# Optimization experiments

Measured on AMD Instinct MI355X. Metric: run time of the kernel, lower is better.

Reference implementation:

```python
import jax, jax.numpy as jnp
import numpy as np

N_EMBD = 1024
N_HEAD = 16
HEAD_DIM = N_EMBD // N_HEAD


def setup_inputs() -> dict:
    key = jax.random.key(0)
    ks = jax.random.split(key, 9)
    B, T, C = 4, 2048, N_EMBD
    s = 1.0 / np.sqrt(C)
    return {
        "x": jax.random.normal(ks[0], (B, T, C), dtype=jnp.float32),
        "Wq": jax.random.normal(ks[1], (C, C), dtype=jnp.float32) * s,
        "bq": jnp.zeros((C,), dtype=jnp.float32),
        "Wk": jax.random.normal(ks[2], (C, C), dtype=jnp.float32) * s,
        "bk": jnp.zeros((C,), dtype=jnp.float32),
        "Wv": jax.random.normal(ks[3], (C, C), dtype=jnp.float32) * s,
        "bv": jnp.zeros((C,), dtype=jnp.float32),
        "Wo": jax.random.normal(ks[4], (C, C), dtype=jnp.float32) * s,
        "bo": jnp.zeros((C,), dtype=jnp.float32),
    }


def reference(x, Wq, bq, Wk, bk, Wv, bv, Wo, bo):
    B, T, C = x.shape
    H, D = N_HEAD, HEAD_DIM
    # torch Linear: y = x @ W.T + b ; here W stored as (in, out) so y = x @ W + b
    q = (x @ Wq + bq).reshape(B, T, H, D).transpose(0, 2, 1, 3)  # [B,H,T,D]
    k = (x @ Wk + bk).reshape(B, T, H, D).transpose(0, 2, 1, 3)
    v = (x @ Wv + bv).reshape(B, T, H, D).transpose(0, 2, 1, 3)
    scores = jnp.einsum('bhqd,bhkd->bhqk', q, k) / jnp.sqrt(jnp.float32(D))
    causal = jnp.tril(jnp.ones((T, T), dtype=bool))  # [T,T]
    scores = jnp.where(causal[None, None, :, :], scores, -jnp.inf)
    weights = jax.nn.softmax(scores, axis=-1)
    # dropout disabled (eval mode / deterministic reference)
    out = jnp.einsum('bhqk,bhkd->bhqd', weights, v)  # [B,H,T,D]
    out = out.transpose(0, 2, 1, 3).reshape(B, T, C)
    return out @ Wo + bo
```

## Files before the change

### kernel.cpp

```cpp
#include <hip/hip_runtime.h>
#include <stdint.h>
#include <stddef.h>

#define NB 4
#define NT 2048
#define NC 1024
#define NH 16
#define ND 64
#define NM (NB*NT)

typedef __bf16 bf16_t;
typedef __attribute__((ext_vector_type(8)))  __bf16 bf16x8;
typedef __attribute__((ext_vector_type(4)))  __bf16 bf16x4;
typedef __attribute__((ext_vector_type(2)))  __bf16 bf16x2;
typedef __attribute__((ext_vector_type(4)))  float  f32x4;
typedef __attribute__((ext_vector_type(16))) float  f32x16;
typedef __attribute__((ext_vector_type(4)))  unsigned int u32x4;

#define QK_SCALE_LOG2E 0.18033688011112042f

__device__ __forceinline__ f32x4 mfma_bf16(bf16x8 a, bf16x8 b, f32x4 c) {
  return __builtin_amdgcn_mfma_f32_16x16x32_bf16(a, b, c, 0, 0, 0);
}
__device__ __forceinline__ f32x16 mfma32(bf16x8 a, bf16x8 b, f32x16 c) {
  return __builtin_amdgcn_mfma_f32_32x32x16_bf16(a, b, c, 0, 0, 0);
}

__device__ __forceinline__ void gld_lds16(const void* g, void* l) {
  __builtin_amdgcn_global_load_lds(
      (const __attribute__((address_space(1))) void*)g,
      (__attribute__((address_space(3))) void*)l, 16, 0, 0);
}

__device__ __forceinline__ unsigned int pack_bf16(float a, float b) {
  bf16x2 t; t[0] = (bf16_t)a; t[1] = (bf16_t)b;
  return __builtin_bit_cast(unsigned int, t);
}

#if __has_builtin(__builtin_amdgcn_permlane32_swap)
typedef __attribute__((ext_vector_type(2))) unsigned int u32x2;
__device__ __forceinline__ void plswap(unsigned int &a, unsigned int &b) {
  u32x2 r = __builtin_amdgcn_permlane32_swap(a, b, false, false);
  a = r[0]; b = r[1];
}
#else
__device__ __forceinline__ void plswap(unsigned int &a, unsigned int &b) {
  asm volatile("s_nop 1\n\tv_permlane32_swap_b32 %0, %1\n\ts_nop 1"
               : "+v"(a), "+v"(b));
}
#endif

__global__ __launch_bounds__(256) void cast_x_kernel(const float* __restrict__ x,
                                                     bf16_t* __restrict__ xb, int n4) {
  const int stride = gridDim.x * blockDim.x;
  for (int i = blockIdx.x * blockDim.x + threadIdx.x; i < n4; i += stride) {
    float4 v = reinterpret_cast<const float4*>(x)[i];
    bf16x4 o;
    o[0] = (bf16_t)v.x; o[1] = (bf16_t)v.y; o[2] = (bf16_t)v.z; o[3] = (bf16_t)v.w;
    reinterpret_cast<bf16x4*>(xb)[i] = o;
  }
}

__global__ __launch_bounds__(256) void wtrans_kernel(
    const float* __restrict__ Wq, const float* __restrict__ Wk,
    const float* __restrict__ Wv, const float* __restrict__ Wo,
    bf16_t* __restrict__ Tq, bf16_t* __restrict__ Tk,
    bf16_t* __restrict__ Tv, bf16_t* __restrict__ To) {
  __shared__ float tile[32][33];
  const int wsel = blockIdx.x >> 10;
  const float* W = (wsel == 0) ? Wq : (wsel == 1) ? Wk : (wsel == 2) ? Wv : Wo;
  bf16_t*     WT = (wsel == 0) ? Tq : (wsel == 1) ? Tk : (wsel == 2) ? Tv : To;
  const int blk = blockIdx.x & 1023;
  const int t = threadIdx.x;
  const int tx = t & 31, ty = t >> 5;
  const int k0 = (blk & 31) << 5;
  const int n0 = (blk >> 5) << 5;
#pragma unroll
  for (int i = 0; i < 4; ++i)
    tile[ty + 8*i][tx] = W[(size_t)(k0 + ty + 8*i)*NC + n0 + tx];
  __syncthreads();
#pragma unroll
  for (int i = 0; i < 4; ++i)
    WT[(size_t)(n0 + ty + 8*i)*NC + k0 + tx] = (bf16_t)tile[tx][ty + 8*i];
}

__global__ __launch_bounds__(256) void vtrans_kernel(const bf16_t* __restrict__ v,
                                                     bf16_t* __restrict__ vt) {
  __shared__ bf16_t tile[64][72];
  const int tid = threadIdx.x;
  const int bh = blockIdx.x >> 5;
  const int t0 = (blockIdx.x & 31) << 6;
  const size_t base = (size_t)bh * (NT * ND);
  {
    const int r = tid >> 2, dc = (tid & 3) << 4;
    const bf16_t* src = v + base + (size_t)(t0 + r)*ND + dc;
    const bf16x8 a = *reinterpret_cast<const bf16x8*>(src);
    const bf16x8 b = *reinterpret_cast<const bf16x8*>(src + 8);
    *reinterpret_cast<bf16x8*>(&tile[r][dc])     = a;
    *reinterpret_cast<bf16x8*>(&tile[r][dc + 8]) = b;
  }
  __syncthreads();
  {
    const int d = tid >> 2, tc = (tid & 3) << 4;
    bf16x8 a, b;
#pragma unroll
    for (int i = 0; i < 8; ++i) { a[i] = tile[tc + i][d]; b[i] = tile[tc + 8 + i][d]; }
    bf16_t* dst = vt + base + (size_t)d*NT + t0 + tc;
    *reinterpret_cast<bf16x8*>(dst)     = a;
    *reinterpret_cast<bf16x8*>(dst + 8) = b;
  }
}

template<int MODE>
__global__ __launch_bounds__(256) void gemm_bt_kernel(
    const bf16_t* __restrict__ A, const bf16_t* __restrict__ BT,
    int M, int N, int K,
    bf16_t* __restrict__ qo, bf16_t* __restrict__ ko, bf16_t* __restrict__ vo,
    const float* __restrict__ b0, const float* __restrict__ b1, const float* __restrict__ b2,
    float* __restrict__ outp, const float* __restrict__ bo)
{
  const int lane = threadIdx.x & 63;
  const int wv = threadIdx.x >> 6;
  const int wr = wv >> 1, wc = wv & 1;
  const int l15 = lane & 15, lg = lane >> 4;
  const int nbn = N >> 7;
  const int bm = blockIdx.x / nbn, bn = blockIdx.x % nbn;
  const int m0 = bm << 7, n0 = bn << 7;

  __shared__ char smem[32768];
  char* As = smem;
  char* Bs = smem + 16384;

  f32x4 acc[4][4] = {};

  const int nkt = K >> 6;
  for (int kt = 0; kt < nkt; ++kt) {
    const int k0 = kt << 6;
    __syncthreads();
#pragma unroll
    for (int i = 0; i < 4; ++i) {
      const int seg = i*4 + wv;
      const int lin = seg*64 + lane;
      const int row = lin >> 3;
      const int ch  = (lin & 7) ^ (row & 7);
      gld_lds16(A  + (size_t)(m0 + row)*K + k0 + (ch << 3), As + seg*1024);
      gld_lds16(BT + (size_t)(n0 + row)*K + k0 + (ch << 3), Bs + seg*1024);
    }
    __syncthreads();
#pragma unroll
    for (int ks = 0; ks < 2; ++ks) {
      bf16x8 af[4], bfr[4];
#pragma unroll
      for (int fr = 0; fr < 4; ++fr) {
        const int row = wr*64 + fr*16 + l15;
        const int ch  = (ks*4 + lg) ^ (row & 7);
        af[fr] = *reinterpret_cast<const bf16x8*>(As + row*128 + ch*16);
      }
#pragma unroll
      for (int fc = 0; fc < 4; ++fc) {
        const int row = wc*64 + fc*16 + l15;
        const int ch  = (ks*4 + lg) ^ (row & 7);
        bfr[fc] = *reinterpret_cast<const bf16x8*>(Bs + row*128 + ch*16);
      }
#pragma unroll
      for (int fr = 0; fr < 4; ++fr)
#pragma unroll
        for (int fc = 0; fc < 4; ++fc)
          acc[fr][fc] = mfma_bf16(af[fr], bfr[fc], acc[fr][fc]);
    }
  }

#pragma unroll
  for (int fr = 0; fr < 4; ++fr) {
#pragma unroll
    for (int fc = 0; fc < 4; ++fc) {
      const int mrow0 = m0 + wr*64 + fr*16 + (lg << 2);
      const int ncol  = n0 + wc*64 + fc*16 + l15;
      if (MODE == 0) {
        const int mat = ncol >> 10, c = ncol & 1023;
        const int h = c >> 6, d = c & 63;
        bf16_t* dst = (mat == 0) ? qo : ((mat == 1) ? ko : vo);
        const float* bptr = (mat == 0) ? b0 : ((mat == 1) ? b1 : b2);
        const float bias = bptr[c];
        const float scl = (mat == 0) ? QK_SCALE_LOG2E : 1.0f;
#pragma unroll
        for (int r = 0; r < 4; ++r) {
          const int mm = mrow0 + r;
          const int bb = mm >> 11, tt = mm & (NT - 1);
          dst[((((size_t)bb*NH + h)*NT + tt) << 6) + d] =
              (bf16_t)((acc[fr][fc][r] + bias) * scl);
        }
      } else {
        const float bias = bo[ncol];
#pragma unroll
        for (int r = 0; r < 4; ++r)
          outp[(size_t)(mrow0 + r)*N + ncol] = acc[fr][fc][r] + bias;
      }
    }
  }
}

__global__ __launch_bounds__(512, 2) void attn_kernel(
    const bf16_t* __restrict__ q, const bf16_t* __restrict__ k, const bf16_t* __restrict__ vt,
    bf16_t* __restrict__ o)
{
  const int tid  = threadIdx.x;
  const int lane = tid & 63;
  const int wv   = tid >> 6;
  const int l31  = lane & 31, h = lane >> 5;

  const int tile = 7 - (blockIdx.x >> 6);
  const int bh   = blockIdx.x & 63;
  const int bb = bh >> 4, hh = bh & 15;
  const int q0 = tile << 8;

  __shared__ char smem[65536];
  char* const ks0 = smem;
  char* const ks1 = smem + 16384;
  char* const vs0 = smem + 32768;
  char* const vs1 = smem + 49152;

  const size_t base = (size_t)bh * (NT * ND);
  const bf16_t* Kg = k  + base;
  const bf16_t* Vg = vt + base;

  const int q0w = q0 + wv*32;
  const int qg  = q0w + l31;

  int offk[2], offv[2], segb[2];
#pragma unroll
  for (int p = 0; p < 2; ++p) {
    const int c = p*512 + tid;
    const int krow = c >> 3;
    const int kch  = (c & 7) ^ (krow & 7);
    offk[p] = krow*ND + (kch << 3);
    const int vrow = c >> 4;
    const int vdc  = (c & 15) ^ (vrow & 15);
    offv[p] = vrow*NT + (vdc << 3);
    segb[p] = (p*8 + wv) << 10;
  }

#pragma unroll
  for (int p = 0; p < 2; ++p) {
    gld_lds16(Kg + offk[p], ks0 + segb[p]);
    gld_lds16(Vg + offv[p], vs0 + segb[p]);
  }

  bf16x8 qf[4];
  {
    const bf16_t* Qg = q + base + (size_t)qg*ND + 8*h;
#pragma unroll
    for (int ds = 0; ds < 4; ++ds)
      qf[ds] = *reinterpret_cast<const bf16x8*>(Qg + 16*ds);
  }

  bf16x8 ones8;
#pragma unroll
  for (int jj = 0; jj < 8; ++jj) ones8[jj] = (bf16_t)1.0f;

  f32x16 oc[2] = {};
  f32x16 lacc = {};

  const int nkv = 2*(tile + 1);

  for (int j = 0; j < nkv; ++j) {
    const bool cur1 = (j & 1) != 0;
    char* const Kc = cur1 ? ks1 : ks0;
    char* const Vc = cur1 ? vs1 : vs0;

    asm volatile("s_waitcnt vmcnt(0)" ::: "memory");
    __builtin_amdgcn_s_barrier();
    __builtin_amdgcn_sched_barrier(0);

    if (j + 1 < nkv) {
      char* const Kn = cur1 ? ks0 : ks1;
      char* const Vn = cur1 ? vs0 : vs1;
      const bf16_t* kp = Kg + (size_t)(j + 1)*(128*ND);
      const bf16_t* vp = Vg + (size_t)(j + 1)*128;
#pragma unroll
      for (int p = 0; p < 2; ++p) {
        gld_lds16(kp + offk[p], Kn + segb[p]);
        gld_lds16(vp + offv[p], Vn + segb[p]);
      }
      __builtin_amdgcn_sched_barrier(0);
    }

    const int ktile0 = j << 7;
#pragma unroll 1
    for (int hf = 0; hf < 2; ++hf) {
      const int kb0 = ktile0 + (hf << 6);
      if (kb0 > q0w + 31) break;

      f32x16 st[2] = {};
      __builtin_amdgcn_s_setprio(1);
#pragma unroll
      for (int ds = 0; ds < 4; ++ds) {
#pragma unroll
        for (int kt = 0; kt < 2; ++kt) {
          const int row = (hf*2 + kt)*32 + l31;
          const int cl  = (2*ds + h) ^ (row & 7);
          const bf16x8 kfr = *reinterpret_cast<const bf16x8*>(Kc + row*128 + cl*16);
          st[kt] = mfma32(kfr, qf[ds], st[kt]);
        }
      }
      __builtin_amdgcn_s_setprio(0);

      if (kb0 + 63 > q0w) {
        const int qrel = qg - kb0 - 4*h;
#pragma unroll
        for (int kt = 0; kt < 2; ++kt)
#pragma unroll
          for (int r = 0; r < 16; ++r) {
            const int kc = (r & 3) + 8*(r >> 2) + 32*kt;
            st[kt][r] = (kc > qrel) ? 0.0f : exp2f(st[kt][r]);
          }
      } else {
#pragma unroll
        for (int kt = 0; kt < 2; ++kt)
#pragma unroll
          for (int r = 0; r < 16; ++r)
            st[kt][r] = exp2f(st[kt][r]);
      }

#pragma unroll
      for (int kt = 0; kt < 2; ++kt) {
#pragma unroll
        for (int g = 0; g < 2; ++g) {
          unsigned int wa = pack_bf16(st[kt][8*g + 0], st[kt][8*g + 1]);
          unsigned int wb = pack_bf16(st[kt][8*g + 2], st[kt][8*g + 3]);
          unsigned int wc = pack_bf16(st[kt][8*g + 4], st[kt][8*g + 5]);
          unsigned int wd = pack_bf16(st[kt][8*g + 6], st[kt][8*g + 7]);
          plswap(wa, wc);
          plswap(wb, wd);
          u32x4 pb; pb[0] = wa; pb[1] = wb; pb[2] = wc; pb[3] = wd;
          const bf16x8 pf = __builtin_bit_cast(bf16x8, pb);
          const int cv = 2*(4*hf + 2*kt + g) + h;
          __builtin_amdgcn_s_setprio(1);
          lacc = mfma32(ones8, pf, lacc);
#pragma unroll
          for (int da = 0; da < 2; ++da) {
            const int row = 32*da + l31;
            const int lcv = cv ^ (row & 15);
            const bf16x8 vf = *reinterpret_cast<const bf16x8*>(Vc + row*256 + lcv*16);
            oc[da] = mfma32(vf, pf, oc[da]);
          }
          __builtin_amdgcn_s_setprio(0);
        }
      }
    }
  }

  const float rl = 1.0f / lacc[0];
  bf16_t* orow = o + ((size_t)bb*NT + qg)*NC + hh*ND;
#pragma unroll
  for (int da = 0; da < 2; ++da) {
#pragma unroll
    for (int u = 0; u < 4; ++u) {
      bf16x4 ov;
#pragma unroll
      for (int jj = 0; jj < 4; ++jj) ov[jj] = (bf16_t)(oc[da][4*u + jj] * rl);
      *reinterpret_cast<bf16x4*>(orow + 32*da + 8*u + 4*h) = ov;
    }
  }
}

extern "C" void kernel_launch(void* const* d_in, const int* in_sizes, int n_in,
                              void* d_out, int out_size, void* d_ws, size_t ws_size,
                              hipStream_t stream) {
  (void)in_sizes; (void)n_in; (void)out_size;
  const float* x  = (const float*)d_in[0];
  const float* Wq = (const float*)d_in[1];
  const float* bq = (const float*)d_in[2];
  const float* Wk = (const float*)d_in[3];
  const float* bk = (const float*)d_in[4];
  const float* Wv = (const float*)d_in[5];
  const float* bv = (const float*)d_in[6];
  const float* Wo = (const float*)d_in[7];
  const float* bo = (const float*)d_in[8];
  float* out = (float*)d_out;

  const size_t off_xb    = 0;
  const size_t off_wqkvT = 16777216;
  const size_t off_woT   = 23068672;
  const size_t off_q     = 25165824;
  const size_t off_k     = 41943040;
  const size_t off_v     = 58720256;
  const size_t off_attn  = 75497472;
  const size_t need      = 92274688;
  if (ws_size < need) return;

  char* ws = (char*)d_ws;
  bf16_t* xb    = (bf16_t*)(ws + off_xb);
  bf16_t* wqkvT = (bf16_t*)(ws + off_wqkvT);
  bf16_t* woT   = (bf16_t*)(ws + off_woT);
  bf16_t* qb    = (bf16_t*)(ws + off_q);
  bf16_t* kb    = (bf16_t*)(ws + off_k);
  bf16_t* vb    = (bf16_t*)(ws + off_v);
  bf16_t* vtb   = (bf16_t*)(ws + off_xb);
  bf16_t* attnb = (bf16_t*)(ws + off_attn);

  cast_x_kernel<<<dim3(2048), dim3(256), 0, stream>>>(x, xb, NM*NC/4);
  wtrans_kernel<<<dim3(4096), dim3(256), 0, stream>>>(
      Wq, Wk, Wv, Wo, wqkvT, wqkvT + 1048576, wqkvT + 2097152, woT);

  gemm_bt_kernel<0><<<dim3(64*24), dim3(256), 0, stream>>>(
      xb, wqkvT, NM, 3*NC, NC, qb, kb, vb, bq, bk, bv, nullptr, nullptr);

  vtrans_kernel<<<dim3(2048), dim3(256), 0, stream>>>(vb, vtb);

  attn_kernel<<<dim3(8*64), dim3(512), 0, stream>>>(qb, kb, vtb, attnb);

  gemm_bt_kernel<1><<<dim3(64*8), dim3(256), 0, stream>>>(
      attnb, woT, NM, NC, NC, nullptr, nullptr, nullptr, nullptr, nullptr, nullptr,
      out, bo);
}
```

Baseline: 178.6 us.

## Shrink attention tiles to 128 queries and 64-key blocks with balanced tile order

The attention kernel now uses 256-thread blocks covering 128 query rows and streams K/V in 64-key blocks, halving shared memory to 32 KB and doubling the grid to 1024 blocks. Tiles are interleaved so short and long causal tiles are paired for better load balance, and the V swizzle is adapted to the narrower block. This is meant to raise occupancy and reduce causal tail imbalance. In exchange there are more barriers and loads per unit of work and less K/V reuse per block.

```diff
diff --git a/kernel.cpp b/kernel.cpp
--- a/kernel.cpp
+++ b/kernel.cpp
@@ -8,6 +8,7 @@
 #define NH 16
 #define ND 64
 #define NM (NB*NT)
+#define KVB 64
 
 typedef __bf16 bf16_t;
 typedef __attribute__((ext_vector_type(8)))  __bf16 bf16x8;
@@ -200,7 +201,7 @@
   }
 }
 
-__global__ __launch_bounds__(512, 2) void attn_kernel(
+__global__ __launch_bounds__(256, 4) void attn_kernel(
     const bf16_t* __restrict__ q, const bf16_t* __restrict__ k, const bf16_t* __restrict__ vt,
     bf16_t* __restrict__ o)
 {
@@ -209,16 +210,19 @@
   const int wv   = tid >> 6;
   const int l31  = lane & 31, h = lane >> 5;
 
-  const int tile = 7 - (blockIdx.x >> 6);
-  const int bh   = blockIdx.x & 63;
+  const int qq = blockIdx.x >> 6;
+  const int quart = qq >> 2, idx = qq & 3;
+  const int tile = (quart & 1) ? (2*idx + (quart >> 1))
+                               : (15 - (quart >> 1) - 2*idx);
+  const int bh = blockIdx.x & 63;
   const int bb = bh >> 4, hh = bh & 15;
-  const int q0 = tile << 8;
-
-  __shared__ char smem[65536];
+  const int q0 = tile << 7;
+
+  __shared__ char smem[32768];
   char* const ks0 = smem;
-  char* const ks1 = smem + 16384;
-  char* const vs0 = smem + 32768;
-  char* const vs1 = smem + 49152;
+  char* const ks1 = smem + 8192;
+  char* const vs0 = smem + 16384;
+  char* const vs1 = smem + 24576;
 
   const size_t base = (size_t)bh * (NT * ND);
   const bf16_t* Kg = k  + base;
@@ -230,14 +234,12 @@
   int offk[2], offv[2], segb[2];
 #pragma unroll
   for (int p = 0; p < 2; ++p) {
-    const int c = p*512 + tid;
-    const int krow = c >> 3;
-    const int kch  = (c & 7) ^ (krow & 7);
-    offk[p] = krow*ND + (kch << 3);
-    const int vrow = c >> 4;
-    const int vdc  = (c & 15) ^ (vrow & 15);
-    offv[p] = vrow*NT + (vdc << 3);
-    segb[p] = (p*8 + wv) << 10;
+    const int c   = p*256 + tid;
+    const int row = c >> 3;
+    const int ch  = (c & 7) ^ (row & 7);
+    offk[p] = row*ND + (ch << 3);
+    offv[p] = row*NT + (ch << 3);
+    segb[p] = (p*4 + wv) << 10;
   }
 
 #pragma unroll
@@ -264,6 +266,7 @@
   const int nkv = 2*(tile + 1);
 
   for (int j = 0; j < nkv; ++j) {
+    const int kt0 = j << 6;
     const bool cur1 = (j & 1) != 0;
     char* const Kc = cur1 ? ks1 : ks0;
     char* const Vc = cur1 ? vs1 : vs0;
@@ -275,8 +278,8 @@
     if (j + 1 < nkv) {
       char* const Kn = cur1 ? ks0 : ks1;
       char* const Vn = cur1 ? vs0 : vs1;
-      const bf16_t* kp = Kg + (size_t)(j + 1)*(128*ND);
-      const bf16_t* vp = Vg + (size_t)(j + 1)*128;
+      const bf16_t* kp = Kg + (size_t)(j + 1)*(KVB*ND);
+      const bf16_t* vp = Vg + (size_t)(j + 1)*KVB;
 #pragma unroll
       for (int p = 0; p < 2; ++p) {
         gld_lds16(kp + offk[p], Kn + segb[p]);
@@ -285,19 +288,14 @@
       __builtin_amdgcn_sched_barrier(0);
     }
 
-    const int ktile0 = j << 7;
-#pragma unroll 1
-    for (int hf = 0; hf < 2; ++hf) {
-      const int kb0 = ktile0 + (hf << 6);
-      if (kb0 > q0w + 31) break;
-
+    if (kt0 <= q0w + 31) {
       f32x16 st[2] = {};
       __builtin_amdgcn_s_setprio(1);
 #pragma unroll
       for (int ds = 0; ds < 4; ++ds) {
 #pragma unroll
         for (int kt = 0; kt < 2; ++kt) {
-          const int row = (hf*2 + kt)*32 + l31;
+          const int row = kt*32 + l31;
           const int cl  = (2*ds + h) ^ (row & 7);
           const bf16x8 kfr = *reinterpret_cast<const bf16x8*>(Kc + row*128 + cl*16);
           st[kt] = mfma32(kfr, qf[ds], st[kt]);
@@ -305,8 +303,8 @@
       }
       __builtin_amdgcn_s_setprio(0);
 
-      if (kb0 + 63 > q0w) {
-        const int qrel = qg - kb0 - 4*h;
+      if (kt0 + KVB - 1 > q0w) {
+        const int qrel = qg - kt0 - 4*h;
 #pragma unroll
         for (int kt = 0; kt < 2; ++kt)
 #pragma unroll
@@ -334,14 +332,14 @@
           plswap(wb, wd);
           u32x4 pb; pb[0] = wa; pb[1] = wb; pb[2] = wc; pb[3] = wd;
           const bf16x8 pf = __builtin_bit_cast(bf16x8, pb);
-          const int cv = 2*(4*hf + 2*kt + g) + h;
+          const int kg = 2*kt + g;
           __builtin_amdgcn_s_setprio(1);
           lacc = mfma32(ones8, pf, lacc);
 #pragma unroll
           for (int da = 0; da < 2; ++da) {
             const int row = 32*da + l31;
-            const int lcv = cv ^ (row & 15);
-            const bf16x8 vf = *reinterpret_cast<const bf16x8*>(Vc + row*256 + lcv*16);
+            const int cl  = (2*kg + h) ^ (row & 7);
+            const bf16x8 vf = *reinterpret_cast<const bf16x8*>(Vc + row*128 + cl*16);
             oc[da] = mfma32(vf, pf, oc[da]);
           }
           __builtin_amdgcn_s_setprio(0);
@@ -358,7 +356,7 @@
     for (int u = 0; u < 4; ++u) {
       bf16x4 ov;
 #pragma unroll
-      for (int jj = 0; jj < 4; ++jj) ov[jj] = (bf16_t)(oc[da][4*u + jj] * rl);
+      for (int jj3 = 0; jj3 < 4; ++jj3) ov[jj3] = (bf16_t)(oc[da][4*u + jj3] * rl);
       *reinterpret_cast<bf16x4*>(orow + 32*da + 8*u + 4*h) = ov;
     }
   }
@@ -408,7 +406,7 @@
 
   vtrans_kernel<<<dim3(2048), dim3(256), 0, stream>>>(vb, vtb);
 
-  attn_kernel<<<dim3(8*64), dim3(512), 0, stream>>>(qb, kb, vtb, attnb);
+  attn_kernel<<<dim3(16*64), dim3(256), 0, stream>>>(qb, kb, vtb, attnb);
 
   gemm_bt_kernel<1><<<dim3(64*8), dim3(256), 0, stream>>>(
       attnb, woT, NM, NC, NC, nullptr, nullptr, nullptr, nullptr, nullptr, nullptr,
```

Result: slower. 210.8 us (+18.0%).
